# Optimization experiments

Hardware: AMD Instinct MI355X
Metric: run time of the kernel (lower is better)

Reference implementation:

```python
import jax, jax.numpy as jnp
import numpy as np

K = 4            # n_factors
AGG_PARAM = 0.5
EPS = 1e-12      # F.normalize eps


def _normalize(v):
    # F.normalize along last axis: v / max(||v||, eps)
    return v / jnp.maximum(jnp.linalg.norm(v, axis=-1, keepdims=True), EPS)


def _aggregate(x, nbrs, max_iter):
    # x: [b, n, d], nbrs: [n, m] with values in [0, n] (n -> zero pad row)
    b, n, d = x.shape
    m = nbrs.shape[-1]
    dd = d // K
    xk = _normalize(x.reshape(b, n, K, dd))            # [b,n,k,dd]
    z_src = jnp.concatenate(
        [xk.reshape(b, n, d), jnp.zeros((b, 1, d), x.dtype)], axis=1)
    z = z_src[:, nbrs.reshape(-1)].reshape(b, n, m, K, dd)  # gather neighbors
    u = None
    for it in range(max_iter):
        if u is None:
            p = jnp.full((b, n, m, K), 1.0 / K, x.dtype)  # softmax of zeros
        else:
            logits = jnp.einsum('bnmkd,bnkd->bnmk', z, u)
            p = jax.nn.softmax(logits, axis=3)
        u = jnp.einsum('bnmkd,bnmk->bnkd', z, p) + xk
        if it < max_iter - 1:
            u = _normalize(u)
    return u.reshape(b, n, d)


def setup_inputs() -> dict:
    key = jax.random.key(0)
    k1, k2 = jax.random.split(key)
    T, b, n, d, m = 3, 1, 50000, 64, 16
    x_all = jax.random.normal(k1, (T, b, n, d), dtype=jnp.float32)
    neighbors_all = jax.random.randint(k2, (T, n, m), 0, n, dtype=jnp.int64)
    return {"x_all": x_all, "neighbors_all": neighbors_all, "max_iter": 3}


def reference(x_all, neighbors_all, max_iter):
    T = x_all.shape[0]
    embs = []
    for t in range(T):
        x_temp = _aggregate(x_all[t], neighbors_all[t], max_iter)
        if t > 0:
            w = jax.nn.sigmoid(
                jnp.arange(t, dtype=x_all.dtype)).reshape(t, 1, 1, 1)
            e = (jnp.sum(w * jnp.stack(embs), axis=0) / t * AGG_PARAM
                 + x_temp * (1.0 - AGG_PARAM))
        else:
            e = x_temp
        embs.append(e)
    return jnp.stack(embs)  # [T, b, n, d]
```

## Files before the change

kernel.cpp:

```cpp
#include <hip/hip_runtime.h>


constexpr int T = 3;
constexpr int N = 50000;
constexpr int D = 64;
constexpr int M = 16;
constexpr float EPS2 = 1e-24f;

template <int CTRL>
__device__ __forceinline__ float dpp_add(float v) {
    int rot = __builtin_amdgcn_mov_dpp(__float_as_int(v), CTRL, 0xF, 0xF, false);
    return v + __int_as_float(rot);
}
__device__ __forceinline__ float rowsum16(float v) {
    v = dpp_add<0x128>(v);
    v = dpp_add<0x124>(v);
    v = dpp_add<0x122>(v);
    v = dpp_add<0x121>(v);
    return v;
}

__global__ __launch_bounds__(256, 4) void eaconv_fused(
    const float* __restrict__ x_all,
    const int*   __restrict__ nbr_all,
    float*       __restrict__ out)
{
    __shared__ float ub[4][D];
    __shared__ float wb[4][D];
    const int wv   = threadIdx.x >> 6;
    const int i    = blockIdx.x * 4 + wv;
    const int lane = threadIdx.x & 63;
    const int p  = lane & 15;
    const int k  = lane >> 4;
    float* uw  = ub[wv];
    float* wwp = wb[wv];
    const int rowb = 64 * k;

    float acc = 0.f;
    const float s1q = 0.25f * 0.7310585786300049f;

#pragma unroll
    for (int t = 0; t < T; ++t) {
        const float* x = x_all + (size_t)t * N * D;
        int j = nbr_all[((size_t)t * N + i) * M + p];
        const bool valid = (unsigned)j < (unsigned)N;
        j = valid ? j : 0;

        float zr[16];
#pragma unroll
        for (int m = 0; m < 16; ++m) {
            const int jm = __builtin_amdgcn_readlane(j, m);
            zr[m] = x[(size_t)jm * D + lane];
        }

        const float* zrp = x + (size_t)j * D + 16 * k;
        const float4 r0 = *(const float4*)(zrp + 0);
        const float4 r1 = *(const float4*)(zrp + 4);
        const float4 r2 = *(const float4*)(zrp + 8);
        const float4 r3 = *(const float4*)(zrp + 12);
        float zrow[16] = {r0.x,r0.y,r0.z,r0.w, r1.x,r1.y,r1.z,r1.w,
                          r2.x,r2.y,r2.z,r2.w, r3.x,r3.y,r3.z,r3.w};

        const float xv = x[(size_t)i * D + lane];
        const float sx = rowsum16(xv * xv);
        const float xh = xv * __builtin_amdgcn_rsqf(fmaxf(sx, EPS2));

        float b0 = zrow[0]*zrow[0], b1 = zrow[1]*zrow[1],
              b2 = zrow[2]*zrow[2], b3 = zrow[3]*zrow[3];
#pragma unroll
        for (int q = 4; q < 16; q += 4) {
            b0 = fmaf(zrow[q+0], zrow[q+0], b0);
            b1 = fmaf(zrow[q+1], zrow[q+1], b1);
            b2 = fmaf(zrow[q+2], zrow[q+2], b2);
            b3 = fmaf(zrow[q+3], zrow[q+3], b3);
        }
        float rz = __builtin_amdgcn_rsqf(fmaxf((b0+b1)+(b2+b3), EPS2));
        if (!valid) rz = 0.f;
#pragma unroll
        for (int q = 0; q < 16; ++q) zrow[q] *= rz;

        wwp[lane] = rz;
        float rzr[16];
        {
            const float4 v0 = *(const float4*)((char*)wwp + rowb);
            const float4 v1 = *(const float4*)((char*)wwp + rowb + 16);
            const float4 v2 = *(const float4*)((char*)wwp + rowb + 32);
            const float4 v3 = *(const float4*)((char*)wwp + rowb + 48);
            rzr[ 0]=v0.x; rzr[ 1]=v0.y; rzr[ 2]=v0.z; rzr[ 3]=v0.w;
            rzr[ 4]=v1.x; rzr[ 5]=v1.y; rzr[ 6]=v1.z; rzr[ 7]=v1.w;
            rzr[ 8]=v2.x; rzr[ 9]=v2.y; rzr[10]=v2.z; rzr[11]=v2.w;
            rzr[12]=v3.x; rzr[13]=v3.y; rzr[14]=v3.z; rzr[15]=v3.w;
        }
#pragma unroll
        for (int m = 0; m < 16; ++m) zr[m] *= rzr[m];

        float t0a = zr[0]+zr[1], t0b = zr[2]+zr[3], t0c = zr[4]+zr[5],
              t0d = zr[6]+zr[7], t0e = zr[8]+zr[9], t0f = zr[10]+zr[11],
              t0g = zr[12]+zr[13], t0h = zr[14]+zr[15];
        float u = fmaf(xh, 4.0f,
                       ((t0a+t0b)+(t0c+t0d)) + ((t0e+t0f)+(t0g+t0h)));
        float inv = __builtin_amdgcn_rsqf(fmaxf(rowsum16(u * u), EPS2));
        uw[lane] = u;

#pragma unroll
        for (int it = 1; it < 3; ++it) {
            float urow[16];
            {
                const float4 v0 = *(const float4*)((char*)uw + rowb);
                const float4 v1 = *(const float4*)((char*)uw + rowb + 16);
                const float4 v2 = *(const float4*)((char*)uw + rowb + 32);
                const float4 v3 = *(const float4*)((char*)uw + rowb + 48);
                urow[ 0]=v0.x; urow[ 1]=v0.y; urow[ 2]=v0.z; urow[ 3]=v0.w;
                urow[ 4]=v1.x; urow[ 5]=v1.y; urow[ 6]=v1.z; urow[ 7]=v1.w;
                urow[ 8]=v2.x; urow[ 9]=v2.y; urow[10]=v2.z; urow[11]=v2.w;
                urow[12]=v3.x; urow[13]=v3.y; urow[14]=v3.z; urow[15]=v3.w;
            }
            float d0 = zrow[0]*urow[0], d1 = zrow[1]*urow[1],
                  d2 = zrow[2]*urow[2], d3 = zrow[3]*urow[3];
#pragma unroll
            for (int q = 4; q < 16; q += 4) {
                d0 = fmaf(zrow[q+0], urow[q+0], d0);
                d1 = fmaf(zrow[q+1], urow[q+1], d1);
                d2 = fmaf(zrow[q+2], urow[q+2], d2);
                d3 = fmaf(zrow[q+3], urow[q+3], d3);
            }
            const float logit = ((d0+d1)+(d2+d3)) * inv;
            const float e = __expf(logit);
            float es = e + __shfl_xor(e, 16, 64);
            es += __shfl_xor(es, 32, 64);
            const float wf = e * __builtin_amdgcn_rcpf(es);

            wwp[lane] = wf;
            float wfr[16];
            {
                const float4 v0 = *(const float4*)((char*)wwp + rowb);
                const float4 v1 = *(const float4*)((char*)wwp + rowb + 16);
                const float4 v2 = *(const float4*)((char*)wwp + rowb + 32);
                const float4 v3 = *(const float4*)((char*)wwp + rowb + 48);
                wfr[ 0]=v0.x; wfr[ 1]=v0.y; wfr[ 2]=v0.z; wfr[ 3]=v0.w;
                wfr[ 4]=v1.x; wfr[ 5]=v1.y; wfr[ 6]=v1.z; wfr[ 7]=v1.w;
                wfr[ 8]=v2.x; wfr[ 9]=v2.y; wfr[10]=v2.z; wfr[11]=v2.w;
                wfr[12]=v3.x; wfr[13]=v3.y; wfr[14]=v3.z; wfr[15]=v3.w;
            }
            u = xh;
#pragma unroll
            for (int m = 0; m < 16; ++m) u = fmaf(wfr[m], zr[m], u);
            if (it < 2) {
                inv = __builtin_amdgcn_rsqf(fmaxf(rowsum16(u * u), EPS2));
                uw[lane] = u;
            }
        }

        float wout;
        if (t == 0)      { wout = u; acc = u; }
        else if (t == 1) { wout = 0.25f * acc + 0.5f * u;
                           acc = fmaf(s1q, wout, 0.125f * acc); }
        else             { wout = acc + 0.5f * u; }
        out[((size_t)t * N + i) * D + lane] = wout;
    }
}

extern "C" void kernel_launch(void* const* d_in, const int* in_sizes, int n_in,
                              void* d_out, int out_size, void* d_ws, size_t ws_size,
                              hipStream_t stream) {
    const float* x_all = (const float*)d_in[0];
    const int*   nbrs  = (const int*)d_in[1];
    float*       out   = (float*)d_out;

    eaconv_fused<<<N / 4, 256, 0, stream>>>(x_all, nbrs, out);
}
```

Baseline: 188.8 us.

## Prefetch next timestep's neighbor gathers during current iteration and fold normalization scale

```diff
diff --git a/kernel.cpp b/kernel.cpp
--- a/kernel.cpp
+++ b/kernel.cpp
@@ -20,7 +20,7 @@
     return v;
 }
 
-__global__ __launch_bounds__(256, 4) void eaconv_fused(
+__global__ __launch_bounds__(256, 3) void eaconv_fused(
     const float* __restrict__ x_all,
     const int*   __restrict__ nbr_all,
     float*       __restrict__ out)
@@ -39,29 +39,36 @@
     float acc = 0.f;
     const float s1q = 0.25f * 0.7310585786300049f;
 
+    int jc = nbr_all[(size_t)i * M + p];
+    bool valid = (unsigned)jc < (unsigned)N;
+    jc = valid ? jc : 0;
+    float xv = x_all[(size_t)i * D + lane];
+    float zr[16];
+#pragma unroll
+    for (int m = 0; m < 16; ++m) {
+        const int jm = __builtin_amdgcn_readlane(jc, m);
+        zr[m] = x_all[(size_t)jm * D + lane];
+    }
+    const float* zrp0 = x_all + (size_t)jc * D + 16 * k;
+    float4 zw0 = *(const float4*)(zrp0 + 0);
+    float4 zw1 = *(const float4*)(zrp0 + 4);
+    float4 zw2 = *(const float4*)(zrp0 + 8);
+    float4 zw3 = *(const float4*)(zrp0 + 12);
+
 #pragma unroll
     for (int t = 0; t < T; ++t) {
-        const float* x = x_all + (size_t)t * N * D;
-        int j = nbr_all[((size_t)t * N + i) * M + p];
-        const bool valid = (unsigned)j < (unsigned)N;
-        j = valid ? j : 0;
-
-        float zr[16];
-#pragma unroll
-        for (int m = 0; m < 16; ++m) {
-            const int jm = __builtin_amdgcn_readlane(j, m);
-            zr[m] = x[(size_t)jm * D + lane];
+        int jn = 0; bool validn = false; float xvn = 0.f;
+        const float* xn = x_all + (size_t)(t + 1) * N * D;
+        if (t < T - 1) {
+            jn = nbr_all[((size_t)(t + 1) * N + i) * M + p];
+            validn = (unsigned)jn < (unsigned)N;
+            jn = validn ? jn : 0;
+            xvn = xn[(size_t)i * D + lane];
         }
 
-        const float* zrp = x + (size_t)j * D + 16 * k;
-        const float4 r0 = *(const float4*)(zrp + 0);
-        const float4 r1 = *(const float4*)(zrp + 4);
-        const float4 r2 = *(const float4*)(zrp + 8);
-        const float4 r3 = *(const float4*)(zrp + 12);
-        float zrow[16] = {r0.x,r0.y,r0.z,r0.w, r1.x,r1.y,r1.z,r1.w,
-                          r2.x,r2.y,r2.z,r2.w, r3.x,r3.y,r3.z,r3.w};
+        float zrow[16] = {zw0.x,zw0.y,zw0.z,zw0.w, zw1.x,zw1.y,zw1.z,zw1.w,
+                          zw2.x,zw2.y,zw2.z,zw2.w, zw3.x,zw3.y,zw3.z,zw3.w};
 
-        const float xv = x[(size_t)i * D + lane];
         const float sx = rowsum16(xv * xv);
         const float xh = xv * __builtin_amdgcn_rsqf(fmaxf(sx, EPS2));
 
@@ -76,31 +83,45 @@
         }
         float rz = __builtin_amdgcn_rsqf(fmaxf((b0+b1)+(b2+b3), EPS2));
         if (!valid) rz = 0.f;
-#pragma unroll
-        for (int q = 0; q < 16; ++q) zrow[q] *= rz;
 
         wwp[lane] = rz;
-        float rzr[16];
+        float wfr[16];
         {
             const float4 v0 = *(const float4*)((char*)wwp + rowb);
             const float4 v1 = *(const float4*)((char*)wwp + rowb + 16);
             const float4 v2 = *(const float4*)((char*)wwp + rowb + 32);
             const float4 v3 = *(const float4*)((char*)wwp + rowb + 48);
-            rzr[ 0]=v0.x; rzr[ 1]=v0.y; rzr[ 2]=v0.z; rzr[ 3]=v0.w;
-            rzr[ 4]=v1.x; rzr[ 5]=v1.y; rzr[ 6]=v1.z; rzr[ 7]=v1.w;
-            rzr[ 8]=v2.x; rzr[ 9]=v2.y; rzr[10]=v2.z; rzr[11]=v2.w;
-            rzr[12]=v3.x; rzr[13]=v3.y; rzr[14]=v3.z; rzr[15]=v3.w;
+            wfr[ 0]=v0.x; wfr[ 1]=v0.y; wfr[ 2]=v0.z; wfr[ 3]=v0.w;
+            wfr[ 4]=v1.x; wfr[ 5]=v1.y; wfr[ 6]=v1.z; wfr[ 7]=v1.w;
+            wfr[ 8]=v2.x; wfr[ 9]=v2.y; wfr[10]=v2.z; wfr[11]=v2.w;
+            wfr[12]=v3.x; wfr[13]=v3.y; wfr[14]=v3.z; wfr[15]=v3.w;
         }
+        float s0 = wfr[0]*zr[0], s1 = wfr[1]*zr[1],
+              s2 = wfr[2]*zr[2], s3 = wfr[3]*zr[3];
 #pragma unroll
-        for (int m = 0; m < 16; ++m) zr[m] *= rzr[m];
-
-        float t0a = zr[0]+zr[1], t0b = zr[2]+zr[3], t0c = zr[4]+zr[5],
-              t0d = zr[6]+zr[7], t0e = zr[8]+zr[9], t0f = zr[10]+zr[11],
-              t0g = zr[12]+zr[13], t0h = zr[14]+zr[15];
-        float u = fmaf(xh, 4.0f,
-                       ((t0a+t0b)+(t0c+t0d)) + ((t0e+t0f)+(t0g+t0h)));
+        for (int q = 4; q < 16; q += 4) {
+            s0 = fmaf(wfr[q+0], zr[q+0], s0);
+            s1 = fmaf(wfr[q+1], zr[q+1], s1);
+            s2 = fmaf(wfr[q+2], zr[q+2], s2);
+            s3 = fmaf(wfr[q+3], zr[q+3], s3);
+        }
+        float u = fmaf(xh, 4.0f, (s0+s1)+(s2+s3));
         float inv = __builtin_amdgcn_rsqf(fmaxf(rowsum16(u * u), EPS2));
         uw[lane] = u;
+
+        float zrn[16]; float4 zn0, zn1, zn2, zn3;
+        if (t < T - 1) {
+#pragma unroll
+            for (int m = 0; m < 16; ++m) {
+                const int jm = __builtin_amdgcn_readlane(jn, m);
+                zrn[m] = xn[(size_t)jm * D + lane];
+            }
+            const float* zrpn = xn + (size_t)jn * D + 16 * k;
+            zn0 = *(const float4*)(zrpn + 0);
+            zn1 = *(const float4*)(zrpn + 4);
+            zn2 = *(const float4*)(zrpn + 8);
+            zn3 = *(const float4*)(zrpn + 12);
+        }
 
 #pragma unroll
         for (int it = 1; it < 3; ++it) {
@@ -124,14 +145,13 @@
                 d2 = fmaf(zrow[q+2], urow[q+2], d2);
                 d3 = fmaf(zrow[q+3], urow[q+3], d3);
             }
-            const float logit = ((d0+d1)+(d2+d3)) * inv;
+            const float logit = ((d0+d1)+(d2+d3)) * (rz * inv);
             const float e = __expf(logit);
             float es = e + __shfl_xor(e, 16, 64);
             es += __shfl_xor(es, 32, 64);
-            const float wf = e * __builtin_amdgcn_rcpf(es);
+            const float wf = e * __builtin_amdgcn_rcpf(es) * rz;
 
             wwp[lane] = wf;
-            float wfr[16];
             {
                 const float4 v0 = *(const float4*)((char*)wwp + rowb);
                 const float4 v1 = *(const float4*)((char*)wwp + rowb + 16);
@@ -157,6 +177,13 @@
                            acc = fmaf(s1q, wout, 0.125f * acc); }
         else             { wout = acc + 0.5f * u; }
         out[((size_t)t * N + i) * D + lane] = wout;
+
+        if (t < T - 1) {
+            jc = jn; valid = validn; xv = xvn;
+#pragma unroll
+            for (int m = 0; m < 16; ++m) zr[m] = zrn[m];
+            zw0 = zn0; zw1 = zn1; zw2 = zn2; zw3 = zn3;
+        }
     }
 }
 
```

Result: faster. 184.7 us (-2.2%).

## Process two nodes per wavefront to raise memory-level parallelism

Applied to the files above, without the earlier changes.

```diff
diff --git a/kernel.cpp b/kernel.cpp
--- a/kernel.cpp
+++ b/kernel.cpp
@@ -20,143 +20,180 @@
     return v;
 }
 
-__global__ __launch_bounds__(256, 4) void eaconv_fused(
+__global__ __launch_bounds__(256, 3) void eaconv_fused(
     const float* __restrict__ x_all,
     const int*   __restrict__ nbr_all,
     float*       __restrict__ out)
 {
-    __shared__ float ub[4][D];
-    __shared__ float wb[4][D];
-    const int wv   = threadIdx.x >> 6;
-    const int i    = blockIdx.x * 4 + wv;
-    const int lane = threadIdx.x & 63;
+    __shared__ float ub[4][2][D];
+    __shared__ float wb[4][2][D];
+    const int wv    = threadIdx.x >> 6;
+    const int ibase = blockIdx.x * 8 + wv * 2;
+    const int lane  = threadIdx.x & 63;
     const int p  = lane & 15;
     const int k  = lane >> 4;
-    float* uw  = ub[wv];
-    float* wwp = wb[wv];
     const int rowb = 64 * k;
 
-    float acc = 0.f;
+    float acc[2] = {0.f, 0.f};
     const float s1q = 0.25f * 0.7310585786300049f;
 
 #pragma unroll
     for (int t = 0; t < T; ++t) {
         const float* x = x_all + (size_t)t * N * D;
-        int j = nbr_all[((size_t)t * N + i) * M + p];
-        const bool valid = (unsigned)j < (unsigned)N;
-        j = valid ? j : 0;
-
-        float zr[16];
-#pragma unroll
-        for (int m = 0; m < 16; ++m) {
-            const int jm = __builtin_amdgcn_readlane(j, m);
-            zr[m] = x[(size_t)jm * D + lane];
-        }
-
-        const float* zrp = x + (size_t)j * D + 16 * k;
-        const float4 r0 = *(const float4*)(zrp + 0);
-        const float4 r1 = *(const float4*)(zrp + 4);
-        const float4 r2 = *(const float4*)(zrp + 8);
-        const float4 r3 = *(const float4*)(zrp + 12);
-        float zrow[16] = {r0.x,r0.y,r0.z,r0.w, r1.x,r1.y,r1.z,r1.w,
-                          r2.x,r2.y,r2.z,r2.w, r3.x,r3.y,r3.z,r3.w};
-
-        const float xv = x[(size_t)i * D + lane];
-        const float sx = rowsum16(xv * xv);
-        const float xh = xv * __builtin_amdgcn_rsqf(fmaxf(sx, EPS2));
-
-        float b0 = zrow[0]*zrow[0], b1 = zrow[1]*zrow[1],
-              b2 = zrow[2]*zrow[2], b3 = zrow[3]*zrow[3];
-#pragma unroll
-        for (int q = 4; q < 16; q += 4) {
-            b0 = fmaf(zrow[q+0], zrow[q+0], b0);
-            b1 = fmaf(zrow[q+1], zrow[q+1], b1);
-            b2 = fmaf(zrow[q+2], zrow[q+2], b2);
-            b3 = fmaf(zrow[q+3], zrow[q+3], b3);
-        }
-        float rz = __builtin_amdgcn_rsqf(fmaxf((b0+b1)+(b2+b3), EPS2));
-        if (!valid) rz = 0.f;
-#pragma unroll
-        for (int q = 0; q < 16; ++q) zrow[q] *= rz;
-
-        wwp[lane] = rz;
-        float rzr[16];
-        {
-            const float4 v0 = *(const float4*)((char*)wwp + rowb);
-            const float4 v1 = *(const float4*)((char*)wwp + rowb + 16);
-            const float4 v2 = *(const float4*)((char*)wwp + rowb + 32);
-            const float4 v3 = *(const float4*)((char*)wwp + rowb + 48);
-            rzr[ 0]=v0.x; rzr[ 1]=v0.y; rzr[ 2]=v0.z; rzr[ 3]=v0.w;
-            rzr[ 4]=v1.x; rzr[ 5]=v1.y; rzr[ 6]=v1.z; rzr[ 7]=v1.w;
-            rzr[ 8]=v2.x; rzr[ 9]=v2.y; rzr[10]=v2.z; rzr[11]=v2.w;
-            rzr[12]=v3.x; rzr[13]=v3.y; rzr[14]=v3.z; rzr[15]=v3.w;
-        }
-#pragma unroll
-        for (int m = 0; m < 16; ++m) zr[m] *= rzr[m];
-
-        float t0a = zr[0]+zr[1], t0b = zr[2]+zr[3], t0c = zr[4]+zr[5],
-              t0d = zr[6]+zr[7], t0e = zr[8]+zr[9], t0f = zr[10]+zr[11],
-              t0g = zr[12]+zr[13], t0h = zr[14]+zr[15];
-        float u = fmaf(xh, 4.0f,
-                       ((t0a+t0b)+(t0c+t0d)) + ((t0e+t0f)+(t0g+t0h)));
-        float inv = __builtin_amdgcn_rsqf(fmaxf(rowsum16(u * u), EPS2));
-        uw[lane] = u;
-
-#pragma unroll
-        for (int it = 1; it < 3; ++it) {
-            float urow[16];
+
+        int   j[2];  bool vld[2];
+        float zr[2][16], zrow[2][16], xh[2], u[2], inv[2], rz[2];
+
+#pragma unroll
+        for (int nn = 0; nn < 2; ++nn) {
+            const int jj = nbr_all[((size_t)t * N + (ibase + nn)) * M + p];
+            vld[nn] = (unsigned)jj < (unsigned)N;
+            j[nn] = vld[nn] ? jj : 0;
+        }
+
+#pragma unroll
+        for (int nn = 0; nn < 2; ++nn) {
+#pragma unroll
+            for (int m = 0; m < 16; ++m) {
+                const int jm = __builtin_amdgcn_readlane(j[nn], m);
+                zr[nn][m] = x[(size_t)jm * D + lane];
+            }
+        }
+
+#pragma unroll
+        for (int nn = 0; nn < 2; ++nn) {
+            const float* zrp = x + (size_t)j[nn] * D + 16 * k;
+            const float4 r0 = *(const float4*)(zrp + 0);
+            const float4 r1 = *(const float4*)(zrp + 4);
+            const float4 r2 = *(const float4*)(zrp + 8);
+            const float4 r3 = *(const float4*)(zrp + 12);
+            zrow[nn][ 0]=r0.x; zrow[nn][ 1]=r0.y; zrow[nn][ 2]=r0.z; zrow[nn][ 3]=r0.w;
+            zrow[nn][ 4]=r1.x; zrow[nn][ 5]=r1.y; zrow[nn][ 6]=r1.z; zrow[nn][ 7]=r1.w;
+            zrow[nn][ 8]=r2.x; zrow[nn][ 9]=r2.y; zrow[nn][10]=r2.z; zrow[nn][11]=r2.w;
+            zrow[nn][12]=r3.x; zrow[nn][13]=r3.y; zrow[nn][14]=r3.z; zrow[nn][15]=r3.w;
+        }
+
+#pragma unroll
+        for (int nn = 0; nn < 2; ++nn) {
+            const float xv = x[(size_t)(ibase + nn) * D + lane];
+            const float sx = rowsum16(xv * xv);
+            xh[nn] = xv * __builtin_amdgcn_rsqf(fmaxf(sx, EPS2));
+        }
+
+#pragma unroll
+        for (int nn = 0; nn < 2; ++nn) {
+            float b0 = zrow[nn][0]*zrow[nn][0], b1 = zrow[nn][1]*zrow[nn][1],
+                  b2 = zrow[nn][2]*zrow[nn][2], b3 = zrow[nn][3]*zrow[nn][3];
+#pragma unroll
+            for (int q = 4; q < 16; q += 4) {
+                b0 = fmaf(zrow[nn][q+0], zrow[nn][q+0], b0);
+                b1 = fmaf(zrow[nn][q+1], zrow[nn][q+1], b1);
+                b2 = fmaf(zrow[nn][q+2], zrow[nn][q+2], b2);
+                b3 = fmaf(zrow[nn][q+3], zrow[nn][q+3], b3);
+            }
+            rz[nn] = __builtin_amdgcn_rsqf(fmaxf((b0+b1)+(b2+b3), EPS2));
+            if (!vld[nn]) rz[nn] = 0.f;
+        }
+
+#pragma unroll
+        for (int nn = 0; nn < 2; ++nn) wb[wv][nn][lane] = rz[nn];
+#pragma unroll
+        for (int nn = 0; nn < 2; ++nn) {
+            float wfr[16];
+            const char* wbase = (const char*)wb[wv][nn] + rowb;
             {
-                const float4 v0 = *(const float4*)((char*)uw + rowb);
-                const float4 v1 = *(const float4*)((char*)uw + rowb + 16);
-                const float4 v2 = *(const float4*)((char*)uw + rowb + 32);
-                const float4 v3 = *(const float4*)((char*)uw + rowb + 48);
-                urow[ 0]=v0.x; urow[ 1]=v0.y; urow[ 2]=v0.z; urow[ 3]=v0.w;
-                urow[ 4]=v1.x; urow[ 5]=v1.y; urow[ 6]=v1.z; urow[ 7]=v1.w;
-                urow[ 8]=v2.x; urow[ 9]=v2.y; urow[10]=v2.z; urow[11]=v2.w;
-                urow[12]=v3.x; urow[13]=v3.y; urow[14]=v3.z; urow[15]=v3.w;
-            }
-            float d0 = zrow[0]*urow[0], d1 = zrow[1]*urow[1],
-                  d2 = zrow[2]*urow[2], d3 = zrow[3]*urow[3];
-#pragma unroll
-            for (int q = 4; q < 16; q += 4) {
-                d0 = fmaf(zrow[q+0], urow[q+0], d0);
-                d1 = fmaf(zrow[q+1], urow[q+1], d1);
-                d2 = fmaf(zrow[q+2], urow[q+2], d2);
-                d3 = fmaf(zrow[q+3], urow[q+3], d3);
-            }
-            const float logit = ((d0+d1)+(d2+d3)) * inv;
-            const float e = __expf(logit);
-            float es = e + __shfl_xor(e, 16, 64);
-            es += __shfl_xor(es, 32, 64);
-            const float wf = e * __builtin_amdgcn_rcpf(es);
-
-            wwp[lane] = wf;
-            float wfr[16];
-            {
-                const float4 v0 = *(const float4*)((char*)wwp + rowb);
-                const float4 v1 = *(const float4*)((char*)wwp + rowb + 16);
-                const float4 v2 = *(const float4*)((char*)wwp + rowb + 32);
-                const float4 v3 = *(const float4*)((char*)wwp + rowb + 48);
+                const float4 v0 = *(const float4*)(wbase);
+                const float4 v1 = *(const float4*)(wbase + 16);
+                const float4 v2 = *(const float4*)(wbase + 32);
+                const float4 v3 = *(const float4*)(wbase + 48);
                 wfr[ 0]=v0.x; wfr[ 1]=v0.y; wfr[ 2]=v0.z; wfr[ 3]=v0.w;
                 wfr[ 4]=v1.x; wfr[ 5]=v1.y; wfr[ 6]=v1.z; wfr[ 7]=v1.w;
                 wfr[ 8]=v2.x; wfr[ 9]=v2.y; wfr[10]=v2.z; wfr[11]=v2.w;
                 wfr[12]=v3.x; wfr[13]=v3.y; wfr[14]=v3.z; wfr[15]=v3.w;
             }
-            u = xh;
-#pragma unroll
-            for (int m = 0; m < 16; ++m) u = fmaf(wfr[m], zr[m], u);
-            if (it < 2) {
-                inv = __builtin_amdgcn_rsqf(fmaxf(rowsum16(u * u), EPS2));
-                uw[lane] = u;
-            }
-        }
-
-        float wout;
-        if (t == 0)      { wout = u; acc = u; }
-        else if (t == 1) { wout = 0.25f * acc + 0.5f * u;
-                           acc = fmaf(s1q, wout, 0.125f * acc); }
-        else             { wout = acc + 0.5f * u; }
-        out[((size_t)t * N + i) * D + lane] = wout;
+            float s0 = wfr[0]*zr[nn][0], s1 = wfr[1]*zr[nn][1],
+                  s2 = wfr[2]*zr[nn][2], s3 = wfr[3]*zr[nn][3];
+#pragma unroll
+            for (int q = 4; q < 16; q += 4) {
+                s0 = fmaf(wfr[q+0], zr[nn][q+0], s0);
+                s1 = fmaf(wfr[q+1], zr[nn][q+1], s1);
+                s2 = fmaf(wfr[q+2], zr[nn][q+2], s2);
+                s3 = fmaf(wfr[q+3], zr[nn][q+3], s3);
+            }
+            u[nn] = fmaf(xh[nn], 4.0f, (s0+s1)+(s2+s3));
+            inv[nn] = __builtin_amdgcn_rsqf(fmaxf(rowsum16(u[nn]*u[nn]), EPS2));
+            ub[wv][nn][lane] = u[nn];
+        }
+
+#pragma unroll
+        for (int it = 1; it < 3; ++it) {
+            float wfv[2];
+#pragma unroll
+            for (int nn = 0; nn < 2; ++nn) {
+                float urow[16];
+                const char* ubase = (const char*)ub[wv][nn] + rowb;
+                {
+                    const float4 v0 = *(const float4*)(ubase);
+                    const float4 v1 = *(const float4*)(ubase + 16);
+                    const float4 v2 = *(const float4*)(ubase + 32);
+                    const float4 v3 = *(const float4*)(ubase + 48);
+                    urow[ 0]=v0.x; urow[ 1]=v0.y; urow[ 2]=v0.z; urow[ 3]=v0.w;
+                    urow[ 4]=v1.x; urow[ 5]=v1.y; urow[ 6]=v1.z; urow[ 7]=v1.w;
+                    urow[ 8]=v2.x; urow[ 9]=v2.y; urow[10]=v2.z; urow[11]=v2.w;
+                    urow[12]=v3.x; urow[13]=v3.y; urow[14]=v3.z; urow[15]=v3.w;
+                }
+                float d0 = zrow[nn][0]*urow[0], d1 = zrow[nn][1]*urow[1],
+                      d2 = zrow[nn][2]*urow[2], d3 = zrow[nn][3]*urow[3];
+#pragma unroll
+                for (int q = 4; q < 16; q += 4) {
+                    d0 = fmaf(zrow[nn][q+0], urow[q+0], d0);
+                    d1 = fmaf(zrow[nn][q+1], urow[q+1], d1);
+                    d2 = fmaf(zrow[nn][q+2], urow[q+2], d2);
+                    d3 = fmaf(zrow[nn][q+3], urow[q+3], d3);
+                }
+                const float logit = ((d0+d1)+(d2+d3)) * (rz[nn] * inv[nn]);
+                const float e = __expf(logit);
+                float es = e + __shfl_xor(e, 16, 64);
+                es += __shfl_xor(es, 32, 64);
+                wfv[nn] = e * __builtin_amdgcn_rcpf(es) * rz[nn];
+            }
+#pragma unroll
+            for (int nn = 0; nn < 2; ++nn) wb[wv][nn][lane] = wfv[nn];
+#pragma unroll
+            for (int nn = 0; nn < 2; ++nn) {
+                float wfr[16];
+                const char* wbase = (const char*)wb[wv][nn] + rowb;
+                {
+                    const float4 v0 = *(const float4*)(wbase);
+                    const float4 v1 = *(const float4*)(wbase + 16);
+                    const float4 v2 = *(const float4*)(wbase + 32);
+                    const float4 v3 = *(const float4*)(wbase + 48);
+                    wfr[ 0]=v0.x; wfr[ 1]=v0.y; wfr[ 2]=v0.z; wfr[ 3]=v0.w;
+                    wfr[ 4]=v1.x; wfr[ 5]=v1.y; wfr[ 6]=v1.z; wfr[ 7]=v1.w;
+                    wfr[ 8]=v2.x; wfr[ 9]=v2.y; wfr[10]=v2.z; wfr[11]=v2.w;
+                    wfr[12]=v3.x; wfr[13]=v3.y; wfr[14]=v3.z; wfr[15]=v3.w;
+                }
+                float uu = xh[nn];
+#pragma unroll
+                for (int m = 0; m < 16; ++m) uu = fmaf(wfr[m], zr[nn][m], uu);
+                u[nn] = uu;
+                if (it < 2) {
+                    inv[nn] = __builtin_amdgcn_rsqf(
+                        fmaxf(rowsum16(uu * uu), EPS2));
+                    ub[wv][nn][lane] = uu;
+                }
+            }
+        }
+
+#pragma unroll
+        for (int nn = 0; nn < 2; ++nn) {
+            float wout;
+            if (t == 0)      { wout = u[nn]; acc[nn] = u[nn]; }
+            else if (t == 1) { wout = 0.25f * acc[nn] + 0.5f * u[nn];
+                               acc[nn] = fmaf(s1q, wout, 0.125f * acc[nn]); }
+            else             { wout = acc[nn] + 0.5f * u[nn]; }
+            out[((size_t)t * N + (ibase + nn)) * D + lane] = wout;
+        }
     }
 }
 
@@ -167,5 +204,5 @@
     const int*   nbrs  = (const int*)d_in[1];
     float*       out   = (float*)d_out;
 
-    eaconv_fused<<<N / 4, 256, 0, stream>>>(x_all, nbrs, out);
-}
+    eaconv_fused<<<N / 8, 256, 0, stream>>>(x_all, nbrs, out);
+}
```

Result: faster. 182.7 us (-3.2%).

## Software-pipeline neighbor gathers across timesteps with double-buffered registers

Applied to the files above, without the earlier changes.

```diff
diff --git a/kernel.cpp b/kernel.cpp
--- a/kernel.cpp
+++ b/kernel.cpp
@@ -20,7 +20,7 @@
     return v;
 }
 
-__global__ __launch_bounds__(256, 4) void eaconv_fused(
+__global__ __launch_bounds__(256, 2) void eaconv_fused(
     const float* __restrict__ x_all,
     const int*   __restrict__ nbr_all,
     float*       __restrict__ out)
@@ -30,41 +30,36 @@
     const int wv   = threadIdx.x >> 6;
     const int i    = blockIdx.x * 4 + wv;
     const int lane = threadIdx.x & 63;
-    const int p  = lane & 15;
-    const int k  = lane >> 4;
+    const int p = lane & 15;
+    const int k = lane >> 4;
     float* uw  = ub[wv];
     float* wwp = wb[wv];
     const int rowb = 64 * k;
 
-    float acc = 0.f;
     const float s1q = 0.25f * 0.7310585786300049f;
 
-#pragma unroll
-    for (int t = 0; t < T; ++t) {
-        const float* x = x_all + (size_t)t * N * D;
-        int j = nbr_all[((size_t)t * N + i) * M + p];
-        const bool valid = (unsigned)j < (unsigned)N;
-        j = valid ? j : 0;
-
-        float zr[16];
+    auto load_z = [&](const float* xs, int j,
+                      float (&zr)[16], float (&zrow)[16]) {
 #pragma unroll
         for (int m = 0; m < 16; ++m) {
             const int jm = __builtin_amdgcn_readlane(j, m);
-            zr[m] = x[(size_t)jm * D + lane];
+            zr[m] = xs[(size_t)jm * D + lane];
         }
-
-        const float* zrp = x + (size_t)j * D + 16 * k;
+        const float* zrp = xs + (size_t)j * D + 16 * k;
         const float4 r0 = *(const float4*)(zrp + 0);
         const float4 r1 = *(const float4*)(zrp + 4);
         const float4 r2 = *(const float4*)(zrp + 8);
         const float4 r3 = *(const float4*)(zrp + 12);
-        float zrow[16] = {r0.x,r0.y,r0.z,r0.w, r1.x,r1.y,r1.z,r1.w,
-                          r2.x,r2.y,r2.z,r2.w, r3.x,r3.y,r3.z,r3.w};
+        zrow[ 0]=r0.x; zrow[ 1]=r0.y; zrow[ 2]=r0.z; zrow[ 3]=r0.w;
+        zrow[ 4]=r1.x; zrow[ 5]=r1.y; zrow[ 6]=r1.z; zrow[ 7]=r1.w;
+        zrow[ 8]=r2.x; zrow[ 9]=r2.y; zrow[10]=r2.z; zrow[11]=r2.w;
+        zrow[12]=r3.x; zrow[13]=r3.y; zrow[14]=r3.z; zrow[15]=r3.w;
+    };
 
-        const float xv = x[(size_t)i * D + lane];
+    auto em = [&](const float (&zr)[16], const float (&zrow)[16],
+                  float xv, bool valid, auto&& prefetch) -> float {
         const float sx = rowsum16(xv * xv);
         const float xh = xv * __builtin_amdgcn_rsqf(fmaxf(sx, EPS2));
-
         float b0 = zrow[0]*zrow[0], b1 = zrow[1]*zrow[1],
               b2 = zrow[2]*zrow[2], b3 = zrow[3]*zrow[3];
 #pragma unroll
@@ -76,31 +71,34 @@
         }
         float rz = __builtin_amdgcn_rsqf(fmaxf((b0+b1)+(b2+b3), EPS2));
         if (!valid) rz = 0.f;
-#pragma unroll
-        for (int q = 0; q < 16; ++q) zrow[q] *= rz;
 
         wwp[lane] = rz;
-        float rzr[16];
+        float wfr[16];
         {
             const float4 v0 = *(const float4*)((char*)wwp + rowb);
             const float4 v1 = *(const float4*)((char*)wwp + rowb + 16);
             const float4 v2 = *(const float4*)((char*)wwp + rowb + 32);
             const float4 v3 = *(const float4*)((char*)wwp + rowb + 48);
-            rzr[ 0]=v0.x; rzr[ 1]=v0.y; rzr[ 2]=v0.z; rzr[ 3]=v0.w;
-            rzr[ 4]=v1.x; rzr[ 5]=v1.y; rzr[ 6]=v1.z; rzr[ 7]=v1.w;
-            rzr[ 8]=v2.x; rzr[ 9]=v2.y; rzr[10]=v2.z; rzr[11]=v2.w;
-            rzr[12]=v3.x; rzr[13]=v3.y; rzr[14]=v3.z; rzr[15]=v3.w;
+            wfr[ 0]=v0.x; wfr[ 1]=v0.y; wfr[ 2]=v0.z; wfr[ 3]=v0.w;
+            wfr[ 4]=v1.x; wfr[ 5]=v1.y; wfr[ 6]=v1.z; wfr[ 7]=v1.w;
+            wfr[ 8]=v2.x; wfr[ 9]=v2.y; wfr[10]=v2.z; wfr[11]=v2.w;
+            wfr[12]=v3.x; wfr[13]=v3.y; wfr[14]=v3.z; wfr[15]=v3.w;
         }
+        float s0 = wfr[0]*zr[0], s1 = wfr[1]*zr[1],
+              s2 = wfr[2]*zr[2], s3 = wfr[3]*zr[3];
 #pragma unroll
-        for (int m = 0; m < 16; ++m) zr[m] *= rzr[m];
-
-        float t0a = zr[0]+zr[1], t0b = zr[2]+zr[3], t0c = zr[4]+zr[5],
-              t0d = zr[6]+zr[7], t0e = zr[8]+zr[9], t0f = zr[10]+zr[11],
-              t0g = zr[12]+zr[13], t0h = zr[14]+zr[15];
-        float u = fmaf(xh, 4.0f,
-                       ((t0a+t0b)+(t0c+t0d)) + ((t0e+t0f)+(t0g+t0h)));
+        for (int q = 4; q < 16; q += 4) {
+            s0 = fmaf(wfr[q+0], zr[q+0], s0);
+            s1 = fmaf(wfr[q+1], zr[q+1], s1);
+            s2 = fmaf(wfr[q+2], zr[q+2], s2);
+            s3 = fmaf(wfr[q+3], zr[q+3], s3);
+        }
+        float u = fmaf(xh, 4.0f, (s0+s1)+(s2+s3));
         float inv = __builtin_amdgcn_rsqf(fmaxf(rowsum16(u * u), EPS2));
         uw[lane] = u;
+
+        prefetch();
+        __builtin_amdgcn_sched_barrier(0);
 
 #pragma unroll
         for (int it = 1; it < 3; ++it) {
@@ -124,14 +122,13 @@
                 d2 = fmaf(zrow[q+2], urow[q+2], d2);
                 d3 = fmaf(zrow[q+3], urow[q+3], d3);
             }
-            const float logit = ((d0+d1)+(d2+d3)) * inv;
+            const float logit = ((d0+d1)+(d2+d3)) * (rz * inv);
             const float e = __expf(logit);
             float es = e + __shfl_xor(e, 16, 64);
             es += __shfl_xor(es, 32, 64);
-            const float wf = e * __builtin_amdgcn_rcpf(es);
+            const float wf = e * __builtin_amdgcn_rcpf(es) * rz;
 
             wwp[lane] = wf;
-            float wfr[16];
             {
                 const float4 v0 = *(const float4*)((char*)wwp + rowb);
                 const float4 v1 = *(const float4*)((char*)wwp + rowb + 16);
@@ -142,22 +139,52 @@
                 wfr[ 8]=v2.x; wfr[ 9]=v2.y; wfr[10]=v2.z; wfr[11]=v2.w;
                 wfr[12]=v3.x; wfr[13]=v3.y; wfr[14]=v3.z; wfr[15]=v3.w;
             }
-            u = xh;
+            float uu = xh;
 #pragma unroll
-            for (int m = 0; m < 16; ++m) u = fmaf(wfr[m], zr[m], u);
+            for (int m = 0; m < 16; ++m) uu = fmaf(wfr[m], zr[m], uu);
+            u = uu;
             if (it < 2) {
                 inv = __builtin_amdgcn_rsqf(fmaxf(rowsum16(u * u), EPS2));
                 uw[lane] = u;
             }
         }
+        return u;
+    };
 
-        float wout;
-        if (t == 0)      { wout = u; acc = u; }
-        else if (t == 1) { wout = 0.25f * acc + 0.5f * u;
-                           acc = fmaf(s1q, wout, 0.125f * acc); }
-        else             { wout = acc + 0.5f * u; }
-        out[((size_t)t * N + i) * D + lane] = wout;
-    }
+    int j0 = nbr_all[(size_t)i * M + p];
+    const bool v0 = (unsigned)j0 < (unsigned)N;
+    j0 = v0 ? j0 : 0;
+    const float xv0 = x_all[(size_t)i * D + lane];
+    float zrA[16], zrowA[16], zrB[16], zrowB[16];
+    load_z(x_all, j0, zrA, zrowA);
+    const int   jr1 = nbr_all[((size_t)N + i) * M + p];
+    const float xv1 = x_all[((size_t)N + i) * D + lane];
+    __builtin_amdgcn_sched_barrier(0);
+
+    bool v1 = false, v2 = false;
+    int jr2 = 0; float xv2 = 0.f;
+
+    float u = em(zrA, zrowA, xv0, v0, [&] {
+        v1 = (unsigned)jr1 < (unsigned)N;
+        const int j1 = v1 ? jr1 : 0;
+        load_z(x_all + (size_t)N * D, j1, zrB, zrowB);
+        jr2 = nbr_all[((size_t)2 * N + i) * M + p];
+        xv2 = x_all[((size_t)2 * N + i) * D + lane];
+    });
+    float acc = u;
+    out[(size_t)i * D + lane] = u;
+
+    u = em(zrB, zrowB, xv1, v1, [&] {
+        v2 = (unsigned)jr2 < (unsigned)N;
+        const int j2 = v2 ? jr2 : 0;
+        load_z(x_all + (size_t)2 * N * D, j2, zrA, zrowA);
+    });
+    const float e1 = 0.25f * acc + 0.5f * u;
+    out[((size_t)N + i) * D + lane] = e1;
+    acc = fmaf(s1q, e1, 0.125f * acc);
+
+    u = em(zrA, zrowA, xv2, v2, [] {});
+    out[((size_t)2 * N + i) * D + lane] = acc + 0.5f * u;
 }
 
 extern "C" void kernel_launch(void* const* d_in, const int* in_sizes, int n_in,
```

Result: faster. 176.2 us (-6.7%).
